# Performance work log

Hardware: AMD Instinct MI355X
Metric: run time of the kernel (lower is better)

## Reference

```python
import jax, jax.numpy as jnp
import numpy as np

B, T, C, H = 8, 2048, 1024, 16
N_LAYER, LAYER_ID = 12, 1
NH = C // H           # head size = 64
CHUNK = 256


def setup_inputs() -> dict:
    key = jax.random.key(0)
    ks = jax.random.split(key, 10)
    # deterministic init matching the torch __init__
    ratio_0_to_1 = LAYER_ID / (N_LAYER - 1)
    ratio_1_to_almost0 = 1.0 - LAYER_ID / N_LAYER
    ddd = np.arange(C, dtype=np.float32) / C
    time_maa_k = (1.0 - ddd ** ratio_1_to_almost0).astype(np.float32)
    time_maa_v = (1.0 - (ddd ** ratio_1_to_almost0 + 0.3 * ratio_0_to_1)).astype(np.float32)
    time_maa_r = (1.0 - ddd ** (0.5 * ratio_1_to_almost0)).astype(np.float32)
    h_idx = np.arange(H, dtype=np.float32)
    time_decay = (-6.0 + 5.0 * (h_idx / (H - 1)) ** (0.7 + 1.3 * ratio_0_to_1)).astype(np.float32)
    s = 0.02
    return {
        "x": jax.random.normal(ks[0], (B, T, C), jnp.float32),
        "volatility": jax.random.uniform(ks[1], (B, T), jnp.float32),
        "Wvol": jax.random.normal(ks[2], (C, 1), jnp.float32) * s,
        "bvol": jnp.zeros((C,), jnp.float32),
        "time_maa_k": jnp.asarray(time_maa_k),
        "time_maa_v": jnp.asarray(time_maa_v),
        "time_maa_r": jnp.asarray(time_maa_r),
        "time_decay": jnp.asarray(time_decay),
        "Wk": jax.random.normal(ks[3], (C, C), jnp.float32) * s,
        "Wv": jax.random.normal(ks[4], (C, C), jnp.float32) * s,
        "Wr": jax.random.normal(ks[5], (C, C), jnp.float32) * s,
        "Wo": jax.random.normal(ks[6], (C, C), jnp.float32) * s,
        "gn_w": 1.0 + jax.random.normal(ks[7], (C,), jnp.float32) * s,
        "gn_b": jax.random.normal(ks[8], (C,), jnp.float32) * s,
    }


def reference(x, volatility, Wvol, bvol, time_maa_k, time_maa_v, time_maa_r,
              time_decay, Wk, Wv, Wr, Wo, gn_w, gn_b):
    b, t, c = x.shape
    h = time_decay.shape[0]
    n = c // h
    nc = t // CHUNK

    # volatility gating: sigmoid(Linear(1->C))
    v_emb = jax.nn.sigmoid(volatility[:, :, None] * Wvol[:, 0] + bvol)  # (B,T,C)
    x = x * v_emb

    # time shift (zero-pad one step at the front, drop last)
    xx = jnp.pad(x, ((0, 0), (1, 0), (0, 0)))[:, :-1] - x
    xk = x + xx * time_maa_k
    xv = x + xx * time_maa_v
    xr = x + xx * time_maa_r

    r = (xr @ Wr.T).reshape(b, t, h, n).transpose(0, 2, 1, 3)  # (B,H,T,N)
    k = (xk @ Wk.T).reshape(b, t, h, n).transpose(0, 2, 1, 3)
    v = (xv @ Wv.T).reshape(b, t, h, n).transpose(0, 2, 1, 3)

    w = jnp.exp(-jnp.exp(time_decay))[None, :, None, None]  # scalar decay per head

    # chunked linear-attention recurrence (faithful to torch loop, chunk=256, no intra-chunk mask)
    rc = r.reshape(b, h, nc, CHUNK, n).transpose(2, 0, 1, 3, 4)  # (nc,B,H,CK,N)
    kc = k.reshape(b, h, nc, CHUNK, n).transpose(2, 0, 1, 3, 4)
    vc = v.reshape(b, h, nc, CHUNK, n).transpose(2, 0, 1, 3, 4)

    def step(state, rkv):
        rr, kk, vv = rkv  # each (B,H,CK,N)
        att = jnp.einsum('bhtn,bhsn->bhts', rr, kk)            # r @ k^T
        y = w * (jnp.einsum('bhts,bhsn->bhtn', att, vv)
                 + jnp.einsum('bhtn,bhnm->bhtm', rr, state))
        new_state = w * (state + jnp.einsum('bhsn,bhsm->bhnm', kk, vv))
        return new_state, y

    state0 = jnp.zeros((b, h, n, n), x.dtype)
    _, ys = jax.lax.scan(step, state0, (rc, kc, vc))            # (nc,B,H,CK,N)
    y = ys.transpose(1, 2, 0, 3, 4).reshape(b, h, t, n)
    y = y.transpose(0, 2, 1, 3).reshape(b * t, c)

    # GroupNorm with H groups over channels
    yg = y.reshape(b * t, h, n)
    mu = yg.mean(-1, keepdims=True)
    var = yg.var(-1, keepdims=True)
    yg = (yg - mu) * jax.lax.rsqrt(var + 1e-5)
    y = (yg.reshape(b * t, c) * gn_w + gn_b).reshape(b, t, c)

    return y @ Wo.T  # dropout is identity in eval
```

## Files before the change

kernel.cpp:

```cpp
#include <hip/hip_runtime.h>

typedef unsigned short u16;
typedef __attribute__((ext_vector_type(4))) unsigned int u32x4;
typedef __attribute__((ext_vector_type(4))) float f32x4;
typedef __attribute__((ext_vector_type(8))) short s16x8;

#define B_ 8
#define T_ 2048
#define C_ 1024
#define H_ 16
#define HS_ 64
#define CHUNK_ 256
#define NC_ 8

union U8 { u32x4 u; u16 h[8]; };

__device__ __forceinline__ float b2f(u16 v) {
    union { unsigned int i; float f; } c; c.i = ((unsigned int)v) << 16; return c.f;
}
__device__ __forceinline__ u16 f2b(float f) {
    union { float f; unsigned int i; } c; c.f = f;
    unsigned int i = c.i;
    return (u16)((i + 0x7FFFu + ((i >> 16) & 1u)) >> 16);
}
__device__ __forceinline__ float fsig(float z) {
    return __builtin_amdgcn_rcpf(1.f + __expf(-z));
}

typedef __attribute__((address_space(1))) void GV;
typedef __attribute__((address_space(3))) void LV;
__device__ __forceinline__ void glds16(const void* g, void* l) {
    __builtin_amdgcn_global_load_lds((GV*)g, (LV*)l, 16, 0, 0);
}

__global__ __launch_bounds__(256) void cvt4_kernel(
    const float* __restrict__ s0, const float* __restrict__ s1,
    const float* __restrict__ s2, const float* __restrict__ s3,
    u16* __restrict__ dst)
{
    int i = blockIdx.x * 256 + threadIdx.x;
    int m = i >> 17;
    const float* s = (m == 0) ? s0 : (m == 1) ? s1 : (m == 2) ? s2 : s3;
    size_t j = (size_t)(i & 131071) * 8;
    f32x4 a = *reinterpret_cast<const f32x4*>(s + j);
    f32x4 b = *reinterpret_cast<const f32x4*>(s + j + 4);
    U8 o;
    #pragma unroll
    for (int k = 0; k < 4; k++) { o.h[k] = f2b(a[k]); o.h[4 + k] = f2b(b[k]); }
    *reinterpret_cast<u32x4*>(dst + (size_t)m * C_ * C_ + j) = o.u;
}

__global__ __launch_bounds__(256) void mix_kernel(
    const float* __restrict__ x, const float* __restrict__ vol,
    const float* __restrict__ Wvol, const float* __restrict__ bvol,
    const float* __restrict__ mk, const float* __restrict__ mv, const float* __restrict__ mr,
    u16* __restrict__ xk, u16* __restrict__ xv, u16* __restrict__ xr)
{
    int idx = blockIdx.x * 256 + threadIdx.x;
    int c0 = (idx & 127) * 8;
    int bt8 = idx >> 7;
    int t0  = (bt8 & 255) * 8;
    int b   = bt8 >> 8;
    size_t rowOff = ((size_t)b * T_ + t0) * C_ + c0;

    float wv[8], bv[8], mkv[8], mvv[8], mrv[8];
    #pragma unroll
    for (int j = 0; j < 8; j += 4) {
        f32x4 a;
        a = *reinterpret_cast<const f32x4*>(Wvol + c0 + j);
        wv[j] = a[0]; wv[j+1] = a[1]; wv[j+2] = a[2]; wv[j+3] = a[3];
        a = *reinterpret_cast<const f32x4*>(bvol + c0 + j);
        bv[j] = a[0]; bv[j+1] = a[1]; bv[j+2] = a[2]; bv[j+3] = a[3];
        a = *reinterpret_cast<const f32x4*>(mk + c0 + j);
        mkv[j] = a[0]; mkv[j+1] = a[1]; mkv[j+2] = a[2]; mkv[j+3] = a[3];
        a = *reinterpret_cast<const f32x4*>(mv + c0 + j);
        mvv[j] = a[0]; mvv[j+1] = a[1]; mvv[j+2] = a[2]; mvv[j+3] = a[3];
        a = *reinterpret_cast<const f32x4*>(mr + c0 + j);
        mrv[j] = a[0]; mrv[j+1] = a[1]; mrv[j+2] = a[2]; mrv[j+3] = a[3];
    }

    const float* volb = vol + (size_t)b * T_;
    float gp[8];
    if (t0 == 0) {
        #pragma unroll
        for (int j = 0; j < 8; j++) gp[j] = 0.f;
    } else {
        float vp = volb[t0 - 1];
        #pragma unroll
        for (int j = 0; j < 8; j += 4) {
            f32x4 a = *reinterpret_cast<const f32x4*>(x + rowOff - C_ + j);
            gp[j]   = a[0] * fsig(vp * wv[j]   + bv[j]);
            gp[j+1] = a[1] * fsig(vp * wv[j+1] + bv[j+1]);
            gp[j+2] = a[2] * fsig(vp * wv[j+2] + bv[j+2]);
            gp[j+3] = a[3] * fsig(vp * wv[j+3] + bv[j+3]);
        }
    }

    #pragma unroll
    for (int s = 0; s < 8; s++) {
        float vc = volb[t0 + s];
        size_t off = rowOff + (size_t)s * C_;
        float g[8];
        #pragma unroll
        for (int j = 0; j < 8; j += 4) {
            f32x4 a = *reinterpret_cast<const f32x4*>(x + off + j);
            g[j]   = a[0] * fsig(vc * wv[j]   + bv[j]);
            g[j+1] = a[1] * fsig(vc * wv[j+1] + bv[j+1]);
            g[j+2] = a[2] * fsig(vc * wv[j+2] + bv[j+2]);
            g[j+3] = a[3] * fsig(vc * wv[j+3] + bv[j+3]);
        }
        U8 ok, ov, orr;
        #pragma unroll
        for (int j = 0; j < 8; j++) {
            float xx = gp[j] - g[j];
            ok.h[j]  = f2b(g[j] + xx * mkv[j]);
            ov.h[j]  = f2b(g[j] + xx * mvv[j]);
            orr.h[j] = f2b(g[j] + xx * mrv[j]);
            gp[j] = g[j];
        }
        *reinterpret_cast<u32x4*>(xk + off) = ok.u;
        *reinterpret_cast<u32x4*>(xv + off) = ov.u;
        *reinterpret_cast<u32x4*>(xr + off) = orr.u;
    }
}

#define GBM_ 256
#define GBN_ 256
#define GBK_ 64
#define GK_  1024
#define GNT_ 16
#define GEMM_LDS_BYTES 131072

template<bool F32OUT>
__global__ __launch_bounds__(512, 2) void gemm_bt(
    const u16* __restrict__ A, const u16* __restrict__ W, void* __restrict__ Cc)
{
    extern __shared__ __align__(16) u16 lds[];
    const int tid  = threadIdx.x;
    const int lane = tid & 63, w = tid >> 6;
    const int r16  = lane & 15, quad = lane >> 4;
    const int wm2  = w >> 2;
    const int wn4  = w & 3;
    const int id   = blockIdx.x;
    const int bm   = id & 63, bn = id >> 6;

    const u16* Ab = A + (size_t)bm * GBM_ * GK_;
    const u16* Wb = W + (size_t)bn * GBN_ * GK_;

    const int srow8  = lane >> 3;
    const int schunk = ((lane & 7) ^ srow8) * 8;
    const u16* aSrc = Ab + (size_t)(w * 16 + srow8) * GK_ + schunk;
    const u16* bSrc = Wb + (size_t)(w * 16 + srow8) * GK_ + schunk;

    const int fA0 = (wm2 * 128 + r16) * 64;
    const int fB0 = 16384 + (wn4 * 64 + r16) * 64;
    const int c0 = ((quad)     ^ (r16 & 7)) * 8;
    const int c1 = ((quad | 4) ^ (r16 & 7)) * 8;

    f32x4 acc[8][4];
    #pragma unroll
    for (int mi = 0; mi < 8; mi++)
        #pragma unroll
        for (int ni = 0; ni < 4; ni++)
            acc[mi][ni] = f32x4{0.f, 0.f, 0.f, 0.f};

#define STQ(tt, h) do {                                                       \
    const size_t ko_ = (size_t)(tt) * 64;                                     \
    u16* db_ = lds + (((tt) & 1) * 32768) + ((h) * 128 + w * 16) * 64;        \
    glds16(aSrc + (size_t)((h) * 128)     * GK_ + ko_, db_);                  \
    glds16(aSrc + (size_t)((h) * 128 + 8) * GK_ + ko_, db_ + 512);            \
    glds16(bSrc + (size_t)((h) * 128)     * GK_ + ko_, db_ + 16384);          \
    glds16(bSrc + (size_t)((h) * 128 + 8) * GK_ + ko_, db_ + 16384 + 512);    \
} while (0)

#define PH_BAR() do { asm volatile("" ::: "memory");                          \
    __builtin_amdgcn_s_barrier(); asm volatile("" ::: "memory"); } while (0)
#define PH_LGKM0() do { asm volatile("s_waitcnt lgkmcnt(0)" ::: "memory");    \
    __builtin_amdgcn_sched_barrier(0); } while (0)
#define LDFA(CO) { _Pragma("unroll") for (int mi = 0; mi < 8; mi++)           \
    fa[mi] = *reinterpret_cast<const s16x8*>(lds + pb + fA0 + mi * 1024 + (CO)); }
#define LDFB(NH, CO) { _Pragma("unroll") for (int ni = 0; ni < 2; ni++)       \
    fb[ni] = *reinterpret_cast<const s16x8*>(lds + pb + fB0 + ((NH) * 2 + ni) * 1024 + (CO)); }
#define MFMA16(NH) do { __builtin_amdgcn_s_setprio(1);                        \
    _Pragma("unroll") for (int mi = 0; mi < 8; mi++) {                        \
        acc[mi][(NH)*2+0] = __builtin_amdgcn_mfma_f32_16x16x32_bf16(          \
            fa[mi], fb[0], acc[mi][(NH)*2+0], 0, 0, 0);                       \
        acc[mi][(NH)*2+1] = __builtin_amdgcn_mfma_f32_16x16x32_bf16(          \
            fa[mi], fb[1], acc[mi][(NH)*2+1], 0, 0, 0);                       \
    } __builtin_amdgcn_s_setprio(0); } while (0)

    STQ(0, 0);
    STQ(0, 1);
    asm volatile("s_waitcnt vmcnt(0)" ::: "memory");
    PH_BAR();

    for (int t = 0; t < GNT_; ++t) {
        const int pb = (t & 1) * 32768;
        s16x8 fa[8], fb[2];
        LDFA(c0); LDFB(0, c0);
        if (t + 1 < GNT_) STQ(t + 1, 0);
        PH_BAR(); PH_LGKM0(); MFMA16(0); PH_BAR();
        LDFB(1, c0);
        PH_BAR(); PH_LGKM0(); MFMA16(1); PH_BAR();
        LDFA(c1); LDFB(0, c1);
        if (t + 1 < GNT_) STQ(t + 1, 1);
        PH_BAR(); PH_LGKM0(); MFMA16(0); PH_BAR();
        LDFB(1, c1);
        PH_BAR(); PH_LGKM0(); MFMA16(1);
        asm volatile("s_waitcnt vmcnt(0)" ::: "memory");
        PH_BAR();
    }
#undef STQ
#undef LDFA
#undef LDFB
#undef MFMA16
#undef PH_LGKM0
#undef PH_BAR

    if constexpr (F32OUT) {
        float* C = (float*)Cc;
        #pragma unroll
        for (int mi = 0; mi < 8; mi++) {
            int row0 = bm * GBM_ + wm2 * 128 + mi * 16 + quad * 4;
            #pragma unroll
            for (int ni = 0; ni < 4; ni++) {
                int col = bn * GBN_ + wn4 * 64 + ni * 16 + r16;
                #pragma unroll
                for (int i = 0; i < 4; i++)
                    C[(size_t)(row0 + i) * C_ + col] = acc[mi][ni][i];
            }
        }
    } else {
        u16* ep = lds + w * 4608;
        u16* C = (u16*)Cc;
        #pragma unroll
        for (int half = 0; half < 2; half++) {
            #pragma unroll
            for (int mi2 = 0; mi2 < 4; mi2++) {
                int mi = half * 4 + mi2;
                #pragma unroll
                for (int ni = 0; ni < 4; ni++)
                    #pragma unroll
                    for (int i = 0; i < 4; i++)
                        ep[(mi2 * 16 + quad * 4 + i) * 72 + ni * 16 + r16] =
                            f2b(acc[mi][ni][i]);
            }
            #pragma unroll
            for (int it = 0; it < 8; it++) {
                int rr = it * 8 + (lane >> 3);
                u32x4 val = *reinterpret_cast<const u32x4*>(ep + rr * 72 + (lane & 7) * 8);
                size_t grow = (size_t)(bm * GBM_ + wm2 * 128 + half * 64 + rr);
                *reinterpret_cast<u32x4*>(
                    C + grow * C_ + bn * GBN_ + wn4 * 64 + (lane & 7) * 8) = val;
            }
        }
    }
}

__global__ __launch_bounds__(256) void kvouter_kernel(
    const u16* __restrict__ k, const u16* __restrict__ v, float* __restrict__ S)
{
    int blk = blockIdx.x;
    int j  = blk & (NC_ - 1);
    int bh = blk >> 3;
    int h = bh & (H_ - 1);
    int b = bh >> 4;
    __shared__ __align__(16) u16 kT[HS_ * 136];
    __shared__ __align__(16) u16 vT[HS_ * 136];
    int tid = threadIdx.x, lane = tid & 63, wave = tid >> 6;
    int r16 = lane & 15, quad = lane >> 4;
    int n0 = (wave >> 1) * 32, m0 = (wave & 1) * 32;
    int a = tid & 7, c8 = a * 8;

    f32x4 acc[2][2];
    #pragma unroll
    for (int ni = 0; ni < 2; ni++)
        #pragma unroll
        for (int mi = 0; mi < 2; mi++)
            acc[ni][mi] = f32x4{0.f, 0.f, 0.f, 0.f};

    size_t base = ((size_t)(b * T_ + j * CHUNK_)) * C_ + h * HS_;
    #pragma unroll
    for (int half = 0; half < 2; half++) {
        size_t hb = base + (size_t)half * 128 * C_;
        #pragma unroll
        for (int i = 0; i < 4; i++) {
            int s = (tid + i * 256) >> 3;
            U8 uk, uv;
            uk.u = *reinterpret_cast<const u32x4*>(k + hb + (size_t)s * C_ + c8);
            uv.u = *reinterpret_cast<const u32x4*>(v + hb + (size_t)s * C_ + c8);
            #pragma unroll
            for (int jj = 0; jj < 8; jj++) {
                int w = jj ^ a;
                kT[(c8 + w) * 136 + s] = uk.h[w];
                vT[(c8 + w) * 136 + s] = uv.h[w];
            }
        }
        __syncthreads();
        #pragma unroll
        for (int ks = 0; ks < 4; ks++) {
            s16x8 fa[2], fb[2];
            #pragma unroll
            for (int ni = 0; ni < 2; ni++)
                fa[ni] = *reinterpret_cast<const s16x8*>(
                    &vT[(n0 + ni * 16 + r16) * 136 + ks * 32 + quad * 8]);
            #pragma unroll
            for (int mi = 0; mi < 2; mi++)
                fb[mi] = *reinterpret_cast<const s16x8*>(
                    &kT[(m0 + mi * 16 + r16) * 136 + ks * 32 + quad * 8]);
            #pragma unroll
            for (int ni = 0; ni < 2; ni++)
                #pragma unroll
                for (int mi = 0; mi < 2; mi++)
                    acc[ni][mi] = __builtin_amdgcn_mfma_f32_16x16x32_bf16(fa[ni], fb[mi], acc[ni][mi], 0, 0, 0);
        }
        __syncthreads();
    }
    float* out = S + (size_t)blk * (HS_ * HS_);
    #pragma unroll
    for (int ni = 0; ni < 2; ni++)
        #pragma unroll
        for (int mi = 0; mi < 2; mi++)
            #pragma unroll
            for (int i = 0; i < 4; i++)
                out[(n0 + ni * 16 + quad * 4 + i) * HS_ + m0 + mi * 16 + r16] = acc[ni][mi][i];
}

__global__ __launch_bounds__(256) void scan_kernel(
    const float* __restrict__ S, const float* __restrict__ td, u16* __restrict__ stT)
{
    int bh = blockIdx.x;
    int h = bh & (H_ - 1);
    float w = expf(-expf(td[h]));
    int tid = threadIdx.x;
    float st[16];
    #pragma unroll
    for (int i = 0; i < 16; i++) st[i] = 0.f;
    for (int c = 0; c < NC_; c++) {
        size_t off = ((size_t)(bh * NC_ + c)) * 4096 + tid * 16;
        const float* sp = S + off;
        #pragma unroll
        for (int i = 0; i < 16; i++) st[i] = w * (st[i] + sp[i]);
        U8 o0, o1;
        #pragma unroll
        for (int i = 0; i < 8; i++) { o0.h[i] = f2b(st[i]); o1.h[i] = f2b(st[8 + i]); }
        *reinterpret_cast<u32x4*>(stT + off)     = o0.u;
        *reinterpret_cast<u32x4*>(stT + off + 8) = o1.u;
    }
}

__global__ __launch_bounds__(256) void rstate_gn_kernel(
    const u16* __restrict__ r, const u16* __restrict__ stT,
    const float* __restrict__ gnw, const float* __restrict__ gnb, u16* __restrict__ ygn)
{
    int blk = blockIdx.x;
    int c  = blk & (NC_ - 1);
    int bh = blk >> 3;
    int h = bh & (H_ - 1);
    int b = bh >> 4;
    __shared__ __align__(16) u16 sT[HS_ * 72];
    int tid = threadIdx.x, lane = tid & 63, wave = tid >> 6;
    int r16 = lane & 15, quad = lane >> 4;

    const u16* sg = stT + (size_t)blk * (HS_ * HS_);
    for (int i = tid; i < 512; i += 256) {
        int n = i >> 3, c8 = (i & 7) * 8;
        *reinterpret_cast<u32x4*>(&sT[n * 72 + c8]) =
            *reinterpret_cast<const u32x4*>(sg + n * HS_ + c8);
    }
    __syncthreads();

    size_t rowBase = (size_t)(b * T_ + c * CHUNK_ + wave * 64);
    f32x4 acc[4][4];
    #pragma unroll
    for (int mi = 0; mi < 4; mi++)
        #pragma unroll
        for (int ni = 0; ni < 4; ni++)
            acc[mi][ni] = f32x4{0.f, 0.f, 0.f, 0.f};

    #pragma unroll
    for (int ks = 0; ks < 2; ks++) {
        int kb = ks * 32 + quad * 8;
        s16x8 fa[4], fb[4];
        #pragma unroll
        for (int mi = 0; mi < 4; mi++)
            fa[mi] = *reinterpret_cast<const s16x8*>(
                r + (rowBase + mi * 16 + r16) * C_ + h * HS_ + kb);
        #pragma unroll
        for (int ni = 0; ni < 4; ni++)
            fb[ni] = *reinterpret_cast<const s16x8*>(&sT[(ni * 16 + r16) * 72 + kb]);
        #pragma unroll
        for (int mi = 0; mi < 4; mi++)
            #pragma unroll
            for (int ni = 0; ni < 4; ni++)
                acc[mi][ni] = __builtin_amdgcn_mfma_f32_16x16x32_bf16(fa[mi], fb[ni], acc[mi][ni], 0, 0, 0);
    }

    float gwv[4], gbv[4];
    #pragma unroll
    for (int ni = 0; ni < 4; ni++) {
        int col = ni * 16 + r16;
        gwv[ni] = gnw[h * HS_ + col];
        gbv[ni] = gnb[h * HS_ + col];
    }
    #pragma unroll
    for (int mi = 0; mi < 4; mi++) {
        float s1[4], s2[4];
        #pragma unroll
        for (int i = 0; i < 4; i++) {
            float s = 0.f, ss = 0.f;
            #pragma unroll
            for (int ni = 0; ni < 4; ni++) {
                float v = acc[mi][ni][i];
                s += v; ss += v * v;
            }
            s1[i] = s; s2[i] = ss;
        }
        #pragma unroll
        for (int d = 1; d < 16; d <<= 1) {
            #pragma unroll
            for (int i = 0; i < 4; i++) {
                s1[i] += __shfl_xor(s1[i], d);
                s2[i] += __shfl_xor(s2[i], d);
            }
        }
        #pragma unroll
        for (int i = 0; i < 4; i++) {
            float mu = s1[i] * (1.f / 64.f);
            float var = s2[i] * (1.f / 64.f) - mu * mu;
            float sc = rsqrtf(var + 1e-5f);
            size_t ob = (rowBase + mi * 16 + quad * 4 + i) * C_ + h * HS_;
            #pragma unroll
            for (int ni = 0; ni < 4; ni++)
                ygn[ob + ni * 16 + r16] = f2b((acc[mi][ni][i] - mu) * sc * gwv[ni] + gbv[ni]);
        }
    }
}

extern "C" void kernel_launch(void* const* d_in, const int* in_sizes, int n_in,
                              void* d_out, int out_size, void* d_ws, size_t ws_size,
                              hipStream_t stream) {
    const float* x    = (const float*)d_in[0];
    const float* vol  = (const float*)d_in[1];
    const float* Wvol = (const float*)d_in[2];
    const float* bvol = (const float*)d_in[3];
    const float* mk   = (const float*)d_in[4];
    const float* mv   = (const float*)d_in[5];
    const float* mr   = (const float*)d_in[6];
    const float* td   = (const float*)d_in[7];
    const float* Wk   = (const float*)d_in[8];
    const float* Wv   = (const float*)d_in[9];
    const float* Wr   = (const float*)d_in[10];
    const float* Wo   = (const float*)d_in[11];
    const float* gnw  = (const float*)d_in[12];
    const float* gnb  = (const float*)d_in[13];
    float* out = (float*)d_out;

    static bool init_attr = []() {
        hipFuncSetAttribute(reinterpret_cast<const void*>(gemm_bt<false>),
                            hipFuncAttributeMaxDynamicSharedMemorySize, GEMM_LDS_BYTES);
        hipFuncSetAttribute(reinterpret_cast<const void*>(gemm_bt<true>),
                            hipFuncAttributeMaxDynamicSharedMemorySize, GEMM_LDS_BYTES);
        return true;
    }();
    (void)init_attr;

    char* ws = (char*)d_ws;
    const size_t SLOT = (size_t)B_ * T_ * C_ * 2;
    u16* xr = (u16*)(ws + 0 * SLOT);
    u16* xk = (u16*)(ws + 1 * SLOT);
    u16* xv = (u16*)(ws + 2 * SLOT);
    u16* rb = (u16*)(ws + 3 * SLOT);
    u16* kb = (u16*)(ws + 0 * SLOT);
    u16* vb = (u16*)(ws + 1 * SLOT);
    float* S   = (float*)(ws + 2 * SLOT);
    u16*   stT = (u16*)  (ws + 2 * SLOT + SLOT / 2);
    u16* ygn = (u16*)(ws + 0 * SLOT);
    u16* wtb = (u16*)(ws + 4 * SLOT);
    u16* wrb = wtb;
    u16* wkb = wrb + (size_t)C_ * C_;
    u16* wvb = wkb + (size_t)C_ * C_;
    u16* wob = wvb + (size_t)C_ * C_;

    cvt4_kernel<<<dim3(4 * (C_ * C_ / 8) / 256), dim3(256), 0, stream>>>(Wr, Wk, Wv, Wo, wtb);

    mix_kernel<<<dim3(1024), dim3(256), 0, stream>>>(
        x, vol, Wvol, bvol, mk, mv, mr, xk, xv, xr);

    gemm_bt<false><<<dim3(256), dim3(512), GEMM_LDS_BYTES, stream>>>(xr, wrb, rb);
    gemm_bt<false><<<dim3(256), dim3(512), GEMM_LDS_BYTES, stream>>>(xk, wkb, kb);
    gemm_bt<false><<<dim3(256), dim3(512), GEMM_LDS_BYTES, stream>>>(xv, wvb, vb);

    kvouter_kernel<<<dim3(B_ * H_ * NC_), dim3(256), 0, stream>>>(kb, vb, S);
    scan_kernel<<<dim3(B_ * H_), dim3(256), 0, stream>>>(S, td, stT);
    rstate_gn_kernel<<<dim3(B_ * H_ * NC_), dim3(256), 0, stream>>>(rb, stT, gnw, gnb, ygn);

    gemm_bt<true><<<dim3(256), dim3(512), GEMM_LDS_BYTES, stream>>>(ygn, wob, out);
}
```

Baseline: 373.8 us.

## Write K/V transposed from GEMM epilogue and fuse kv-outer with scan

The K and V projection GEMMs now write their outputs in a channel-major (transposed) layout through a swizzled LDS epilogue. This lets a new fused kernel read MFMA operands straight from global memory and carry the decayed state across chunks in registers, replacing the separate kv-outer and scan kernels. That removes the fp32 S buffer round trip and one launch. The cost is transposed global stores with a 32KB row stride in the GEMM and a scan kernel with only 256 blocks and serial chunk dependence.

After: 339.4 us. -9.2%, faster.

```diff
diff --git a/kernel.cpp b/kernel.cpp
--- a/kernel.cpp
+++ b/kernel.cpp
@@ -131,7 +131,7 @@
 #define GNT_ 16
 #define GEMM_LDS_BYTES 131072
 
-template<bool F32OUT>
+template<int MODE>
 __global__ __launch_bounds__(512, 2) void gemm_bt(
     const u16* __restrict__ A, const u16* __restrict__ W, void* __restrict__ Cc)
 {
@@ -217,7 +217,7 @@
 #undef PH_LGKM0
 #undef PH_BAR
 
-    if constexpr (F32OUT) {
+    if constexpr (MODE == 0) {
         float* C = (float*)Cc;
         #pragma unroll
         for (int mi = 0; mi < 8; mi++) {
@@ -230,7 +230,7 @@
                     C[(size_t)(row0 + i) * C_ + col] = acc[mi][ni][i];
             }
         }
-    } else {
+    } else if constexpr (MODE == 1) {
         u16* ep = lds + w * 4608;
         u16* C = (u16*)Cc;
         #pragma unroll
@@ -245,6 +245,8 @@
                         ep[(mi2 * 16 + quad * 4 + i) * 72 + ni * 16 + r16] =
                             f2b(acc[mi][ni][i]);
             }
+            asm volatile("s_waitcnt lgkmcnt(0)" ::: "memory");
+            __builtin_amdgcn_sched_barrier(0);
             #pragma unroll
             for (int it = 0; it < 8; it++) {
                 int rr = it * 8 + (lane >> 3);
@@ -253,99 +255,85 @@
                 *reinterpret_cast<u32x4*>(
                     C + grow * C_ + bn * GBN_ + wn4 * 64 + (lane & 7) * 8) = val;
             }
-        }
-    }
-}
-
-__global__ __launch_bounds__(256) void kvouter_kernel(
-    const u16* __restrict__ k, const u16* __restrict__ v, float* __restrict__ S)
+            asm volatile("s_waitcnt vmcnt(0) lgkmcnt(0)" ::: "memory");
+        }
+    } else {
+        u16* ep = lds + w * 8192;
+        #pragma unroll
+        for (int mi = 0; mi < 8; mi++) {
+            const int chunk = mi * 2 + (quad >> 1);
+            const int rsub = (quad & 1) * 4;
+            #pragma unroll
+            for (int ni = 0; ni < 4; ni++) {
+                const int col = ni * 16 + r16;
+                u16* p = ep + col * 128 + ((chunk ^ col) & 15) * 8 + rsub;
+                p[0] = f2b(acc[mi][ni][0]);
+                p[1] = f2b(acc[mi][ni][1]);
+                p[2] = f2b(acc[mi][ni][2]);
+                p[3] = f2b(acc[mi][ni][3]);
+            }
+        }
+        asm volatile("s_waitcnt lgkmcnt(0)" ::: "memory");
+        __builtin_amdgcn_sched_barrier(0);
+        u16* C = (u16*)Cc;
+        const int cl = lane >> 2, ch4 = lane & 3;
+        #pragma unroll
+        for (int it = 0; it < 16; it++) {
+            const int col_l = (it & 3) * 16 + cl;
+            const int chunk = (it >> 2) * 4 + ch4;
+            u32x4 val = *reinterpret_cast<const u32x4*>(
+                ep + col_l * 128 + ((chunk ^ col_l) & 15) * 8);
+            const size_t gcol = (size_t)(bn * GBN_ + wn4 * 64 + col_l);
+            const size_t grow = (size_t)(bm * GBM_ + wm2 * 128 + chunk * 8);
+            *reinterpret_cast<u32x4*>(C + gcol * 16384 + grow) = val;
+        }
+    }
+}
+
+__global__ __launch_bounds__(256) void kvscan_kernel(
+    const u16* __restrict__ kT, const u16* __restrict__ vT,
+    const float* __restrict__ td, u16* __restrict__ stT)
 {
-    int blk = blockIdx.x;
-    int j  = blk & (NC_ - 1);
-    int bh = blk >> 3;
-    int h = bh & (H_ - 1);
-    int b = bh >> 4;
-    __shared__ __align__(16) u16 kT[HS_ * 136];
-    __shared__ __align__(16) u16 vT[HS_ * 136];
-    int tid = threadIdx.x, lane = tid & 63, wave = tid >> 6;
-    int r16 = lane & 15, quad = lane >> 4;
-    int n0 = (wave >> 1) * 32, m0 = (wave & 1) * 32;
-    int a = tid & 7, c8 = a * 8;
-
-    f32x4 acc[2][2];
-    #pragma unroll
-    for (int ni = 0; ni < 2; ni++)
-        #pragma unroll
-        for (int mi = 0; mi < 2; mi++)
-            acc[ni][mi] = f32x4{0.f, 0.f, 0.f, 0.f};
-
-    size_t base = ((size_t)(b * T_ + j * CHUNK_)) * C_ + h * HS_;
-    #pragma unroll
-    for (int half = 0; half < 2; half++) {
-        size_t hb = base + (size_t)half * 128 * C_;
-        #pragma unroll
-        for (int i = 0; i < 4; i++) {
-            int s = (tid + i * 256) >> 3;
-            U8 uk, uv;
-            uk.u = *reinterpret_cast<const u32x4*>(k + hb + (size_t)s * C_ + c8);
-            uv.u = *reinterpret_cast<const u32x4*>(v + hb + (size_t)s * C_ + c8);
-            #pragma unroll
-            for (int jj = 0; jj < 8; jj++) {
-                int w = jj ^ a;
-                kT[(c8 + w) * 136 + s] = uk.h[w];
-                vT[(c8 + w) * 136 + s] = uv.h[w];
-            }
-        }
-        __syncthreads();
-        #pragma unroll
-        for (int ks = 0; ks < 4; ks++) {
-            s16x8 fa[2], fb[2];
-            #pragma unroll
-            for (int ni = 0; ni < 2; ni++)
-                fa[ni] = *reinterpret_cast<const s16x8*>(
-                    &vT[(n0 + ni * 16 + r16) * 136 + ks * 32 + quad * 8]);
-            #pragma unroll
-            for (int mi = 0; mi < 2; mi++)
-                fb[mi] = *reinterpret_cast<const s16x8*>(
-                    &kT[(m0 + mi * 16 + r16) * 136 + ks * 32 + quad * 8]);
-            #pragma unroll
-            for (int ni = 0; ni < 2; ni++)
-                #pragma unroll
-                for (int mi = 0; mi < 2; mi++)
-                    acc[ni][mi] = __builtin_amdgcn_mfma_f32_16x16x32_bf16(fa[ni], fb[mi], acc[ni][mi], 0, 0, 0);
-        }
-        __syncthreads();
-    }
-    float* out = S + (size_t)blk * (HS_ * HS_);
-    #pragma unroll
-    for (int ni = 0; ni < 2; ni++)
-        #pragma unroll
-        for (int mi = 0; mi < 2; mi++)
+    const int bm2 = blockIdx.x;
+    const int mh = bm2 & 1, bh = bm2 >> 1;
+    const int h = bh & (H_ - 1), b = bh >> 4;
+    const float wdec = expf(-expf(td[h]));
+    const int tid = threadIdx.x, lane = tid & 63, wave = tid >> 6;
+    const int r16 = lane & 15, quad = lane >> 4;
+    const int n0 = wave * 16;
+
+    const size_t tb = (size_t)b * T_ + quad * 8;
+    const u16* vr  = vT + (size_t)(h * HS_ + n0 + r16) * 16384 + tb;
+    const u16* kr0 = kT + (size_t)(h * HS_ + mh * 32 + r16) * 16384 + tb;
+    const u16* kr1 = kr0 + (size_t)16 * 16384;
+
+    f32x4 st[2];
+    st[0] = f32x4{0.f, 0.f, 0.f, 0.f};
+    st[1] = f32x4{0.f, 0.f, 0.f, 0.f};
+
+    for (int j = 0; j < NC_; j++) {
+        f32x4 acc[2];
+        acc[0] = f32x4{0.f, 0.f, 0.f, 0.f};
+        acc[1] = f32x4{0.f, 0.f, 0.f, 0.f};
+        const int jb = j * CHUNK_;
+        #pragma unroll
+        for (int ks = 0; ks < 8; ks++) {
+            const int co = jb + ks * 32;
+            s16x8 fa  = *reinterpret_cast<const s16x8*>(vr  + co);
+            s16x8 fb0 = *reinterpret_cast<const s16x8*>(kr0 + co);
+            s16x8 fb1 = *reinterpret_cast<const s16x8*>(kr1 + co);
+            acc[0] = __builtin_amdgcn_mfma_f32_16x16x32_bf16(fa, fb0, acc[0], 0, 0, 0);
+            acc[1] = __builtin_amdgcn_mfma_f32_16x16x32_bf16(fa, fb1, acc[1], 0, 0, 0);
+        }
+        u16* out = stT + ((size_t)bh * NC_ + j) * 4096;
+        #pragma unroll
+        for (int mi = 0; mi < 2; mi++) {
+            st[mi] = (st[mi] + acc[mi]) * wdec;
             #pragma unroll
             for (int i = 0; i < 4; i++)
-                out[(n0 + ni * 16 + quad * 4 + i) * HS_ + m0 + mi * 16 + r16] = acc[ni][mi][i];
-}
-
-__global__ __launch_bounds__(256) void scan_kernel(
-    const float* __restrict__ S, const float* __restrict__ td, u16* __restrict__ stT)
-{
-    int bh = blockIdx.x;
-    int h = bh & (H_ - 1);
-    float w = expf(-expf(td[h]));
-    int tid = threadIdx.x;
-    float st[16];
-    #pragma unroll
-    for (int i = 0; i < 16; i++) st[i] = 0.f;
-    for (int c = 0; c < NC_; c++) {
-        size_t off = ((size_t)(bh * NC_ + c)) * 4096 + tid * 16;
-        const float* sp = S + off;
-        #pragma unroll
-        for (int i = 0; i < 16; i++) st[i] = w * (st[i] + sp[i]);
-        U8 o0, o1;
-        #pragma unroll
-        for (int i = 0; i < 8; i++) { o0.h[i] = f2b(st[i]); o1.h[i] = f2b(st[8 + i]); }
-        *reinterpret_cast<u32x4*>(stT + off)     = o0.u;
-        *reinterpret_cast<u32x4*>(stT + off + 8) = o1.u;
+                out[(n0 + quad * 4 + i) * HS_ + mh * 32 + mi * 16 + r16] =
+                    f2b(st[mi][i]);
+        }
     }
 }
 
@@ -457,9 +445,11 @@
     float* out = (float*)d_out;
 
     static bool init_attr = []() {
-        hipFuncSetAttribute(reinterpret_cast<const void*>(gemm_bt<false>),
+        hipFuncSetAttribute(reinterpret_cast<const void*>(gemm_bt<0>),
                             hipFuncAttributeMaxDynamicSharedMemorySize, GEMM_LDS_BYTES);
-        hipFuncSetAttribute(reinterpret_cast<const void*>(gemm_bt<true>),
+        hipFuncSetAttribute(reinterpret_cast<const void*>(gemm_bt<1>),
+                            hipFuncAttributeMaxDynamicSharedMemorySize, GEMM_LDS_BYTES);
+        hipFuncSetAttribute(reinterpret_cast<const void*>(gemm_bt<2>),
                             hipFuncAttributeMaxDynamicSharedMemorySize, GEMM_LDS_BYTES);
         return true;
     }();
@@ -471,10 +461,9 @@
     u16* xk = (u16*)(ws + 1 * SLOT);
     u16* xv = (u16*)(ws + 2 * SLOT);
     u16* rb = (u16*)(ws + 3 * SLOT);
-    u16* kb = (u16*)(ws + 0 * SLOT);
-    u16* vb = (u16*)(ws + 1 * SLOT);
-    float* S   = (float*)(ws + 2 * SLOT);
-    u16*   stT = (u16*)  (ws + 2 * SLOT + SLOT / 2);
+    u16* kbT = (u16*)(ws + 0 * SLOT);
+    u16* vbT = (u16*)(ws + 1 * SLOT);
+    u16* stT = (u16*)(ws + 2 * SLOT + SLOT / 2);
     u16* ygn = (u16*)(ws + 0 * SLOT);
     u16* wtb = (u16*)(ws + 4 * SLOT);
     u16* wrb = wtb;
@@ -487,13 +476,13 @@
     mix_kernel<<<dim3(1024), dim3(256), 0, stream>>>(
         x, vol, Wvol, bvol, mk, mv, mr, xk, xv, xr);
 
-    gemm_bt<false><<<dim3(256), dim3(512), GEMM_LDS_BYTES, stream>>>(xr, wrb, rb);
-    gemm_bt<false><<<dim3(256), dim3(512), GEMM_LDS_BYTES, stream>>>(xk, wkb, kb);
-    gemm_bt<false><<<dim3(256), dim3(512), GEMM_LDS_BYTES, stream>>>(xv, wvb, vb);
-
-    kvouter_kernel<<<dim3(B_ * H_ * NC_), dim3(256), 0, stream>>>(kb, vb, S);
-    scan_kernel<<<dim3(B_ * H_), dim3(256), 0, stream>>>(S, td, stT);
+    gemm_bt<1><<<dim3(256), dim3(512), GEMM_LDS_BYTES, stream>>>(xr, wrb, rb);
+    gemm_bt<2><<<dim3(256), dim3(512), GEMM_LDS_BYTES, stream>>>(xk, wkb, kbT);
+    gemm_bt<2><<<dim3(256), dim3(512), GEMM_LDS_BYTES, stream>>>(xv, wvb, vbT);
+
+    kvscan_kernel<<<dim3(B_ * H_ * 2), dim3(256), 0, stream>>>(kbT, vbT, td, stT);
+
     rstate_gn_kernel<<<dim3(B_ * H_ * NC_), dim3(256), 0, stream>>>(rb, stT, gnw, gnb, ygn);
 
-    gemm_bt<true><<<dim3(256), dim3(512), GEMM_LDS_BYTES, stream>>>(ygn, wob, out);
-}
+    gemm_bt<0><<<dim3(256), dim3(512), GEMM_LDS_BYTES, stream>>>(ygn, wob, out);
+}
```
